# Kernel optimization log

Measured on AMD Instinct MI355X. Metric: run time of the kernel, lower is better.

The kernel has to match this reference:

```python
import jax, jax.numpy as jnp
import numpy as np


def setup_inputs() -> dict:
    key = jax.random.key(0)
    ks = jax.random.split(key, 9)
    B, T, F_IN = 128, 2048, 32
    R, H, F_OUT = 256, 256, 32
    s = lambda k, shape, fan: jax.random.normal(k, shape, dtype=jnp.float32) * (1.0 / np.sqrt(fan))
    return {
        "input_seq": jax.random.normal(ks[0], (B, T, F_IN), dtype=jnp.float32),
        "enc_W": s(ks[1], (R, F_IN), F_IN),
        "enc_b": s(ks[2], (R,), F_IN),
        "W_ih": s(ks[3], (4 * H, R), H),
        "W_hh": s(ks[4], (4 * H, H), H),
        "b_ih": s(ks[5], (4 * H,), H),
        "b_hh": s(ks[6], (4 * H,), H),
        "dec_W": s(ks[7], (F_OUT, H), H),
        "dec_b": s(ks[8], (F_OUT,), H),
        "future_n": 64,
    }


def reference(input_seq, enc_W, enc_b, W_ih, W_hh, b_ih, b_hh, dec_W, dec_b, future_n):
    # Faithful to source: `state` is never updated inside the loop, so every
    # timestep applies the LSTMCell to the SAME initial state (eval: zeros).
    B, T, _ = input_seq.shape
    H = W_hh.shape[1]
    h0 = jnp.zeros((B, H), dtype=input_seq.dtype)
    c0 = jnp.zeros((B, H), dtype=input_seq.dtype)

    encoded = jnp.einsum('btf,rf->btr', input_seq, enc_W) + enc_b  # [B,T,R]
    # future steps all reuse the last encoded timestep
    last = jnp.broadcast_to(encoded[:, -1:, :], (B, future_n, encoded.shape[-1]))
    enc_full = jnp.concatenate([encoded, last], axis=1)  # [B, T+future_n, R]

    # LSTMCell gates (PyTorch order: i, f, g, o); state contribution is constant.
    state_gates = h0 @ W_hh.T + b_hh  # [B, 4H] (zeros state -> just b_hh)
    gates = jnp.einsum('btr,gr->btg', enc_full, W_ih) + b_ih + state_gates[:, None, :]
    i, f, g, o = jnp.split(gates, 4, axis=-1)
    c = jax.nn.sigmoid(f) * c0[:, None, :] + jax.nn.sigmoid(i) * jnp.tanh(g)
    h = jax.nn.sigmoid(o) * jnp.tanh(c)  # [B, T+future_n, H]

    return jnp.einsum('bth,oh->bto', h, dec_W) + dec_b
```

## Files before the change

### kernel.cpp

```cpp
#include <hip/hip_runtime.h>


typedef _Float16 f16x8 __attribute__((ext_vector_type(8)));
typedef _Float16 f16x4 __attribute__((ext_vector_type(4)));
typedef _Float16 f16x2 __attribute__((ext_vector_type(2)));
typedef float    f32x4 __attribute__((ext_vector_type(4)));
typedef float    f32x2 __attribute__((ext_vector_type(2)));
typedef __fp16   h16x2 __attribute__((ext_vector_type(2)));

#define T_IN 2048
#define TT   2112
#define FIN  32
#define FOUT 32

#define WS_FB_OFF   49152
#define WS_DECW_OFF 52224

union PkU { h16x2 h; f16x2 f; unsigned u; };

__global__ __launch_bounds__(256) void prep2(
    const float* __restrict__ enc_W, const float* __restrict__ enc_b,
    const float* __restrict__ W_ih, const float* __restrict__ b_ih,
    const float* __restrict__ b_hh, const float* __restrict__ dec_W,
    _Float16* __restrict__ Mb, float* __restrict__ fb, _Float16* __restrict__ decWb) {
    const int blk = blockIdx.x;
    const int tid = threadIdx.x;
    if (blk < 768) {
        const int gg = blk, sg = gg + (gg >= 256 ? 256 : 0);
        const float SCL = (gg >= 256 && gg < 512) ?  2.8853900817779268f
                                                  : -1.4426950408889634f;
        const float* wr = W_ih + (size_t)sg * 256;
        const int f = tid & 31, r8 = tid >> 5;
        float acc = 0.f;
#pragma unroll
        for (int k = 0; k < 32; ++k) {
            int r = r8 * 32 + k;
            acc = fmaf(wr[r], enc_W[r * 32 + f], acc);
        }
        __shared__ float red[256];
        __shared__ float redb[256];
        __shared__ float red2[32];
        red[tid]  = acc;
        redb[tid] = wr[tid] * enc_b[tid];
        __syncthreads();
        if (tid < 32) {
            float s = 0.f;
#pragma unroll
            for (int k = 0; k < 8; ++k) s += red[k * 32 + tid];
            Mb[gg * 32 + tid] = (_Float16)(s * SCL);
        } else if (tid >= 128 && tid < 160) {
            int t2 = tid - 128;
            float s2 = 0.f;
#pragma unroll
            for (int k = 0; k < 8; ++k) s2 += redb[t2 * 8 + k];
            red2[t2] = s2;
        }
        __syncthreads();
        if (tid == 0) {
            float t = b_ih[sg] + b_hh[sg];
#pragma unroll
            for (int k = 0; k < 32; ++k) t += red2[k];
            fb[gg] = t * SCL;
        }
    } else {
        int i = (blk - 768) * 1024 + tid * 4;
        f32x4 v = *(const f32x4*)(dec_W + i);
        f16x4 o;
#pragma unroll
        for (int j = 0; j < 4; ++j) o[j] = (_Float16)v[j];
        *(f16x4*)(decWb + i) = o;
    }
}

__device__ __forceinline__ unsigned act_pair(f32x2 iv, f32x2 gv, f32x2 ov) {
    f32x2 U, E, Uo;
    U.x  = __builtin_amdgcn_exp2f(iv.x); U.y  = __builtin_amdgcn_exp2f(iv.y);
    E.x  = __builtin_amdgcn_exp2f(gv.x); E.y  = __builtin_amdgcn_exp2f(gv.y);
    Uo.x = __builtin_amdgcn_exp2f(ov.x); Uo.y = __builtin_amdgcn_exp2f(ov.y);
    f32x2 aU = U + 1.0f, aE = E + 1.0f, aUo = Uo + 1.0f;
    f32x2 rU, rE, rUo;
    rU.x  = __builtin_amdgcn_rcpf(aU.x);  rU.y  = __builtin_amdgcn_rcpf(aU.y);
    rE.x  = __builtin_amdgcn_rcpf(aE.x);  rE.y  = __builtin_amdgcn_rcpf(aE.y);
    rUo.x = __builtin_amdgcn_rcpf(aUo.x); rUo.y = __builtin_amdgcn_rcpf(aUo.y);
    f32x2 th = 1.0f - 2.0f * rE;
    f32x2 c  = th * rU;
    PkU cu; cu.h = __builtin_amdgcn_cvt_pkrtz(c.x, c.y);
    PkU su; su.h = __builtin_amdgcn_cvt_pkrtz(rUo.x, rUo.y);
    f16x2 c16 = cu.f, so = su.f;
    f16x2 z  = c16 * c16;
    f16x2 cz = c16 * z;
    f16x2 P  = z * (_Float16)(-5.70498872745e-3f) + (_Float16)(2.06390887954e-2f);
    P = z * P + (_Float16)(-5.37397155531e-2f);
    P = z * P + (_Float16)(1.33314422036e-1f);
    P = z * P + (_Float16)(-3.33332819422e-1f);
    f16x2 tc = cz * P + c16;
    PkU r; r.f = so * tc;
    return r.u;
}

__global__ __launch_bounds__(256) void lstm_main(
    const float* __restrict__ in, const _Float16* __restrict__ Mb,
    const float* __restrict__ fb, const _Float16* __restrict__ decWb,
    const float* __restrict__ dec_b, float* __restrict__ out) {
    __shared__ _Float16 hbuf[4][2][16 * 40];

    const int lane = threadIdx.x & 63;
    const int w    = threadIdx.x >> 6;
    const int l16  = lane & 15;
    const int q    = lane >> 4;
    const int wave = blockIdx.x * 4 + w;
    const int b    = wave >> 6;
    const int t0   = (wave & 63) * 32;

    f16x8 bfr[2];
#pragma unroll
    for (int s = 0; s < 2; ++s) {
        int t  = t0 + s * 16 + l16;
        const float* p = in + ((size_t)(b * T_IN + t)) * FIN + q * 8;
        f32x4 u0 = *(const f32x4*)(p);
        f32x4 u1 = *(const f32x4*)(p + 4);
        f16x8 v;
#pragma unroll
        for (int j = 0; j < 4; ++j) { v[j] = (_Float16)u0[j]; v[4 + j] = (_Float16)u1[j]; }
        bfr[s] = v;
    }

    f32x4 dacc[2][2];
#pragma unroll
    for (int ot = 0; ot < 2; ++ot) {
        f32x4 db = *(const f32x4*)(dec_b + ot * 16 + q * 4);
        dacc[0][ot] = db; dacc[1][ot] = db;
    }

    for (int hc = 0; hc < 8; ++hc) {
        const int hb = hc * 32;
        f16x8 afr[3][2];
        f32x4 fbv[3][2];
#pragma unroll
        for (int gt = 0; gt < 3; ++gt)
#pragma unroll
            for (int X = 0; X < 2; ++X) {
                int grow = gt * 256 + hb + X * 16;
                afr[gt][X] = *(const f16x8*)(Mb + (size_t)(grow + l16) * 32 + q * 8);
                fbv[gt][X] = *(const f32x4*)(fb + grow + q * 4);
            }
        f16x8 a2[2];
#pragma unroll
        for (int ot = 0; ot < 2; ++ot)
            a2[ot] = *(const f16x8*)(decWb + (size_t)(ot * 16 + l16) * 256 + hb + q * 8);

#pragma unroll
        for (int s = 0; s < 2; ++s) {
            f32x4 gi[2], gg[2], go[2];
#pragma unroll
            for (int X = 0; X < 2; ++X) {
                gi[X] = __builtin_amdgcn_mfma_f32_16x16x32_f16(afr[0][X], bfr[s], fbv[0][X], 0, 0, 0);
                gg[X] = __builtin_amdgcn_mfma_f32_16x16x32_f16(afr[1][X], bfr[s], fbv[1][X], 0, 0, 0);
                go[X] = __builtin_amdgcn_mfma_f32_16x16x32_f16(afr[2][X], bfr[s], fbv[2][X], 0, 0, 0);
            }
            _Float16* hp = &hbuf[w][s][0];
#pragma unroll
            for (int X = 0; X < 2; ++X) {
                f32x2 i01 = { gi[X][0], gi[X][1] }, i23 = { gi[X][2], gi[X][3] };
                f32x2 g01 = { gg[X][0], gg[X][1] }, g23 = { gg[X][2], gg[X][3] };
                f32x2 o01 = { go[X][0], go[X][1] }, o23 = { go[X][2], go[X][3] };
                uint2 wv;
                wv.x = act_pair(i01, g01, o01);
                wv.y = act_pair(i23, g23, o23);
                *(uint2*)(hp + l16 * 40 + X * 16 + q * 4) = wv;
            }
            asm volatile("s_waitcnt lgkmcnt(0)" ::: "memory");
            f16x8 b2 = *(const f16x8*)(hp + l16 * 40 + q * 8);
#pragma unroll
            for (int ot = 0; ot < 2; ++ot)
                dacc[s][ot] = __builtin_amdgcn_mfma_f32_16x16x32_f16(a2[ot], b2, dacc[s][ot], 0, 0, 0);
        }
    }

#pragma unroll
    for (int s = 0; s < 2; ++s) {
        int t = t0 + s * 16 + l16;
        size_t ro = ((size_t)(b * TT + t)) * FOUT;
#pragma unroll
        for (int ot = 0; ot < 2; ++ot)
            *(f32x4*)(out + ro + ot * 16 + q * 4) = dacc[s][ot];
    }

    if ((wave & 63) == 63) {
        float* fo = (float*)&hbuf[w][0][0];
        if (l16 == 15) {
            *(f32x4*)(fo + q * 4)      = dacc[1][0];
            *(f32x4*)(fo + 16 + q * 4) = dacc[1][1];
        }
        asm volatile("s_waitcnt lgkmcnt(0)" ::: "memory");
        f32x4 r0 = *(const f32x4*)(fo + q * 4);
        f32x4 r1 = *(const f32x4*)(fo + 16 + q * 4);
#pragma unroll
        for (int fg = 0; fg < 4; ++fg) {
            int t = T_IN + fg * 16 + l16;
            size_t ro = ((size_t)(b * TT + t)) * FOUT;
            *(f32x4*)(out + ro + q * 4)      = r0;
            *(f32x4*)(out + ro + 16 + q * 4) = r1;
        }
    }
}

extern "C" void kernel_launch(void* const* d_in, const int* in_sizes, int n_in,
                              void* d_out, int out_size, void* d_ws, size_t ws_size,
                              hipStream_t stream) {
    const float* input = (const float*)d_in[0];
    const float* enc_W = (const float*)d_in[1];
    const float* enc_b = (const float*)d_in[2];
    const float* W_ih  = (const float*)d_in[3];
    const float* b_ih  = (const float*)d_in[5];
    const float* b_hh  = (const float*)d_in[6];
    const float* dec_W = (const float*)d_in[7];
    const float* dec_b = (const float*)d_in[8];

    _Float16* Mb    = (_Float16*)d_ws;
    float*    fb    = (float*)((char*)d_ws + WS_FB_OFF);
    _Float16* decWb = (_Float16*)((char*)d_ws + WS_DECW_OFF);
    float*    out   = (float*)d_out;

    prep2<<<776, 256, 0, stream>>>(enc_W, enc_b, W_ih, b_ih, b_hh, dec_W, Mb, fb, decWb);
    lstm_main<<<2048, 256, 0, stream>>>(input, Mb, fb, decWb, dec_b, out);
}
```

Baseline: 152.1 us.

## Software-pipeline LDS h readback and decoder MFMA across sub-tiles

Restructures the per-chunk loop so the LDS readback of one sub-tile's h values and its decoder MFMA are deferred and overlapped with the gate MFMAs and activations of the next sub-tile, carrying the previous chunk's decoder weights across iterations. The explicit lgkmcnt(0) wait between each LDS write and readback is removed, relying on the compiler to insert the needed waits. The goal is to hide LDS latency and keep the MFMA pipe busy. It adds register pressure for the carried decoder fragments and relies on wave-local LDS ordering for correctness.

```diff
diff --git a/kernel.cpp b/kernel.cpp
--- a/kernel.cpp
+++ b/kernel.cpp
@@ -132,6 +132,12 @@
         dacc[0][ot] = db; dacc[1][ot] = db;
     }
 
+    _Float16* hp0 = &hbuf[w][0][0];
+    _Float16* hp1 = &hbuf[w][1][0];
+    const int rdoff = l16 * 40 + q * 8;
+
+    f16x8 a2p[2];
+
     for (int hc = 0; hc < 8; ++hc) {
         const int hb = hc * 32;
         f16x8 afr[3][2];
@@ -144,21 +150,21 @@
                 afr[gt][X] = *(const f16x8*)(Mb + (size_t)(grow + l16) * 32 + q * 8);
                 fbv[gt][X] = *(const f32x4*)(fb + grow + q * 4);
             }
-        f16x8 a2[2];
+        f16x8 a2c[2];
 #pragma unroll
         for (int ot = 0; ot < 2; ++ot)
-            a2[ot] = *(const f16x8*)(decWb + (size_t)(ot * 16 + l16) * 256 + hb + q * 8);
-
-#pragma unroll
-        for (int s = 0; s < 2; ++s) {
+            a2c[ot] = *(const f16x8*)(decWb + (size_t)(ot * 16 + l16) * 256 + hb + q * 8);
+
+        {
             f32x4 gi[2], gg[2], go[2];
 #pragma unroll
             for (int X = 0; X < 2; ++X) {
-                gi[X] = __builtin_amdgcn_mfma_f32_16x16x32_f16(afr[0][X], bfr[s], fbv[0][X], 0, 0, 0);
-                gg[X] = __builtin_amdgcn_mfma_f32_16x16x32_f16(afr[1][X], bfr[s], fbv[1][X], 0, 0, 0);
-                go[X] = __builtin_amdgcn_mfma_f32_16x16x32_f16(afr[2][X], bfr[s], fbv[2][X], 0, 0, 0);
-            }
-            _Float16* hp = &hbuf[w][s][0];
+                gi[X] = __builtin_amdgcn_mfma_f32_16x16x32_f16(afr[0][X], bfr[0], fbv[0][X], 0, 0, 0);
+                gg[X] = __builtin_amdgcn_mfma_f32_16x16x32_f16(afr[1][X], bfr[0], fbv[1][X], 0, 0, 0);
+                go[X] = __builtin_amdgcn_mfma_f32_16x16x32_f16(afr[2][X], bfr[0], fbv[2][X], 0, 0, 0);
+            }
+            f16x8 b2;
+            if (hc > 0) b2 = *(const f16x8*)(hp1 + rdoff);
 #pragma unroll
             for (int X = 0; X < 2; ++X) {
                 f32x2 i01 = { gi[X][0], gi[X][1] }, i23 = { gi[X][2], gi[X][3] };
@@ -167,14 +173,48 @@
                 uint2 wv;
                 wv.x = act_pair(i01, g01, o01);
                 wv.y = act_pair(i23, g23, o23);
-                *(uint2*)(hp + l16 * 40 + X * 16 + q * 4) = wv;
-            }
-            asm volatile("s_waitcnt lgkmcnt(0)" ::: "memory");
-            f16x8 b2 = *(const f16x8*)(hp + l16 * 40 + q * 8);
+                *(uint2*)(hp0 + l16 * 40 + X * 16 + q * 4) = wv;
+            }
+            if (hc > 0) {
+#pragma unroll
+                for (int ot = 0; ot < 2; ++ot)
+                    dacc[1][ot] = __builtin_amdgcn_mfma_f32_16x16x32_f16(a2p[ot], b2, dacc[1][ot], 0, 0, 0);
+            }
+        }
+
+        {
+            f32x4 gi[2], gg[2], go[2];
+#pragma unroll
+            for (int X = 0; X < 2; ++X) {
+                gi[X] = __builtin_amdgcn_mfma_f32_16x16x32_f16(afr[0][X], bfr[1], fbv[0][X], 0, 0, 0);
+                gg[X] = __builtin_amdgcn_mfma_f32_16x16x32_f16(afr[1][X], bfr[1], fbv[1][X], 0, 0, 0);
+                go[X] = __builtin_amdgcn_mfma_f32_16x16x32_f16(afr[2][X], bfr[1], fbv[2][X], 0, 0, 0);
+            }
+            f16x8 b2 = *(const f16x8*)(hp0 + rdoff);
+#pragma unroll
+            for (int X = 0; X < 2; ++X) {
+                f32x2 i01 = { gi[X][0], gi[X][1] }, i23 = { gi[X][2], gi[X][3] };
+                f32x2 g01 = { gg[X][0], gg[X][1] }, g23 = { gg[X][2], gg[X][3] };
+                f32x2 o01 = { go[X][0], go[X][1] }, o23 = { go[X][2], go[X][3] };
+                uint2 wv;
+                wv.x = act_pair(i01, g01, o01);
+                wv.y = act_pair(i23, g23, o23);
+                *(uint2*)(hp1 + l16 * 40 + X * 16 + q * 4) = wv;
+            }
 #pragma unroll
             for (int ot = 0; ot < 2; ++ot)
-                dacc[s][ot] = __builtin_amdgcn_mfma_f32_16x16x32_f16(a2[ot], b2, dacc[s][ot], 0, 0, 0);
-        }
+                dacc[0][ot] = __builtin_amdgcn_mfma_f32_16x16x32_f16(a2c[ot], b2, dacc[0][ot], 0, 0, 0);
+        }
+
+#pragma unroll
+        for (int ot = 0; ot < 2; ++ot) a2p[ot] = a2c[ot];
+    }
+
+    {
+        f16x8 b2 = *(const f16x8*)(hp1 + rdoff);
+#pragma unroll
+        for (int ot = 0; ot < 2; ++ot)
+            dacc[1][ot] = __builtin_amdgcn_mfma_f32_16x16x32_f16(a2p[ot], b2, dacc[1][ot], 0, 0, 0);
     }
 
 #pragma unroll
```

New measurement: 155.5 us. +2.2%, slower.
